# Kernel optimization log

Measured on AMD Instinct MI355X. Metric: run time of the kernel, lower is better.

## Reference

```python
import jax, jax.numpy as jnp
import numpy as np

B = 4096
FEAT = 40960
HID = 1024
L1 = 64
L2 = 32
P_ACTIVE = 30.0 / FEAT  # ~30 active features per position


def setup_inputs() -> dict:
    key = jax.random.key(0)
    ks = jax.random.split(key, 12)
    # Sparse binary HalfKP-style features
    white_features = (jax.random.uniform(ks[0], (B, FEAT)) < P_ACTIVE).astype(jnp.float32)
    black_features = (jax.random.uniform(ks[1], (B, FEAT)) < P_ACTIVE).astype(jnp.float32)
    stm = (jax.random.uniform(ks[2], (B, 1)) < 0.5).astype(jnp.float32)
    s = 0.02
    params = {
        'ft_w': jax.random.normal(ks[3], (HID, FEAT), jnp.float32) * s,
        'ft_b': jax.random.normal(ks[4], (HID,), jnp.float32) * s,
        'l1_w': jax.random.normal(ks[5], (L1, 2 * HID), jnp.float32) * s,
        'l1_b': jax.random.normal(ks[6], (L1,), jnp.float32) * s,
        'l2_w': jax.random.normal(ks[7], (L2, L1), jnp.float32) * s,
        'l2_b': jax.random.normal(ks[8], (L2,), jnp.float32) * s,
        'l3_w': jax.random.normal(ks[9], (1, L2), jnp.float32) * s,
        'l3_b': jax.random.normal(ks[10], (1,), jnp.float32) * s,
    }
    return dict(white_features=white_features, black_features=black_features, stm=stm, **params)


def reference(white_features, black_features, stm,
              ft_w, ft_b, l1_w, l1_b, l2_w, l2_b, l3_w, l3_b):
    # Feature transformer (shared weights, both perspectives)
    w = white_features @ ft_w.T + ft_b  # [B, HID]
    b = black_features @ ft_w.T + ft_b  # [B, HID]
    wb = jnp.concatenate([w, b], axis=1)  # [B, 2*HID]
    bw = jnp.concatenate([b, w], axis=1)
    acc = stm * wb + (1.0 - stm) * bw
    h1 = jnp.clip(acc, 0.0, 1.0)
    h2 = jnp.clip(h1 @ l1_w.T + l1_b, 0.0, 1.0)
    h3 = jnp.clip(h2 @ l2_w.T + l2_b, 0.0, 1.0)
    raw = h3 @ l3_w.T + l3_b  # [B, 1]
    return jax.nn.sigmoid(raw), raw
```

## Files before the change

### kernel.cpp

```cpp
#include <hip/hip_runtime.h>
#include <hip/hip_bf16.h>

#define B_SZ 4096
#define FEAT 40960
#define HID  1024
#define L1N  64
#define L2N  32
#define IDX_CAP 128
#define ROWS 4

static __device__ __forceinline__ unsigned short f2bf(float x) {
    __hip_bfloat16 h = __float2bfloat16(x);
    return *reinterpret_cast<unsigned short*>(&h);
}
static __device__ __forceinline__ float bf2f(unsigned short u) {
    unsigned int v = ((unsigned int)u) << 16;
    return __uint_as_float(v);
}
static __device__ __forceinline__ float bf2f_lo(unsigned int u) {
    return __uint_as_float(u << 16);
}
static __device__ __forceinline__ float bf2f_hi(unsigned int u) {
    return __uint_as_float(u & 0xffff0000u);
}
static __device__ __forceinline__ unsigned int packbf(float lo, float hi) {
    return (unsigned int)f2bf(lo) | ((unsigned int)f2bf(hi) << 16);
}
static __device__ __forceinline__ float clipf(float x) {
    return fminf(fmaxf(x, 0.0f), 1.0f);
}

__global__ __launch_bounds__(256) void transpose_ftw(
    const float* __restrict__ ftw, unsigned short* __restrict__ ftwT) {
    __shared__ float tile[32][65];
    const int tx = threadIdx.x;
    const int ty = threadIdx.y;
    const int f0 = blockIdx.x * 32;
    const int h0 = blockIdx.y * 64;
#pragma unroll
    for (int i = 0; i < 8; ++i) {
        int h = ty + 8 * i;
        tile[tx][h] = ftw[(size_t)(h0 + h) * FEAT + f0 + tx];
    }
    __syncthreads();
#pragma unroll
    for (int i = 0; i < 4; ++i) {
        int f = ty + 8 * i;
        unsigned int pk = packbf(tile[f][2 * tx], tile[f][2 * tx + 1]);
        ((unsigned int*)(ftwT + (size_t)(f0 + f) * HID + h0))[tx] = pk;
    }
}

__global__ __launch_bounds__(256) void scan_kernel(
    const float* __restrict__ wf, const float* __restrict__ bfeat,
    int* __restrict__ idx_ws, int* __restrict__ cnt_ws) {
    __shared__ int cnt;
    const int t = threadIdx.x;
    const int b = blockIdx.x;
    const int persp = b >> 12;
    const int row   = b & (B_SZ - 1);
    const float4* s4 = (const float4*)((persp ? bfeat : wf) + (size_t)row * FEAT);
    int* dst = idx_ws + (size_t)b * IDX_CAP;

    if (t == 0) cnt = 0;
    __syncthreads();

#pragma unroll 4
    for (int it = 0; it < (FEAT / 4) / 256; ++it) {
        int i4 = it * 256 + t;
        float4 v = s4[i4];
        int base = i4 * 4;
        if (v.x != 0.f) { int p = atomicAdd(&cnt, 1); if (p < IDX_CAP) dst[p] = base + 0; }
        if (v.y != 0.f) { int p = atomicAdd(&cnt, 1); if (p < IDX_CAP) dst[p] = base + 1; }
        if (v.z != 0.f) { int p = atomicAdd(&cnt, 1); if (p < IDX_CAP) dst[p] = base + 2; }
        if (v.w != 0.f) { int p = atomicAdd(&cnt, 1); if (p < IDX_CAP) dst[p] = base + 3; }
    }
    __syncthreads();
    if (t == 0) cnt_ws[b] = min(cnt, IDX_CAP);
}

__global__ __launch_bounds__(256) void gather_mlp(
    const float* __restrict__ stm, const unsigned short* __restrict__ ftwT,
    const float* __restrict__ ftb,
    const int* __restrict__ idx_ws, const int* __restrict__ cnt_ws,
    const float* __restrict__ l1w, const float* __restrict__ l1b,
    const float* __restrict__ l2w, const float* __restrict__ l2b,
    const float* __restrict__ l3w, const float* __restrict__ l3b,
    float* __restrict__ out) {

    __shared__ int idxs[2 * ROWS][IDX_CAP];
    __shared__ int cnts[2 * ROWS];
    __shared__ unsigned int h1p[ROWS][HID];
    __shared__ float4 part[4 * L1N];
    __shared__ float h2s[ROWS][L1N];
    __shared__ float h3s[ROWS][L2N];

    const int t = threadIdx.x;
    const int r0 = blockIdx.x * ROWS;

    if (t < 2 * ROWS) {
        int pp = t >> 2, r = t & 3;
        cnts[t] = cnt_ws[pp * B_SZ + r0 + r];
    }
    for (int i = t; i < 2 * ROWS * IDX_CAP; i += 256) {
        int l = i >> 7;
        int pp = l >> 2, r = l & 3;
        idxs[l][i & (IDX_CAP - 1)] =
            idx_ws[(size_t)(pp * B_SZ + r0 + r) * IDX_CAP + (i & (IDX_CAP - 1))];
    }
    __syncthreads();

    float4 bias = ((const float4*)ftb)[t];
    float acc[2][ROWS][4];
#pragma unroll
    for (int pp = 0; pp < 2; ++pp)
#pragma unroll
        for (int r = 0; r < ROWS; ++r) {
            acc[pp][r][0] = bias.x; acc[pp][r][1] = bias.y;
            acc[pp][r][2] = bias.z; acc[pp][r][3] = bias.w;
        }

#pragma unroll
    for (int pp = 0; pp < 2; ++pp)
#pragma unroll
        for (int r = 0; r < ROWS; ++r) {
            const int n = cnts[pp * ROWS + r];
            float* a = acc[pp][r];
#pragma unroll 4
            for (int i = 0; i < n; ++i) {
                int f = idxs[pp * ROWS + r][i];
                ushort4 u = ((const ushort4*)(ftwT + (size_t)f * HID))[t];
                a[0] += bf2f(u.x); a[1] += bf2f(u.y);
                a[2] += bf2f(u.z); a[3] += bf2f(u.w);
            }
        }

#pragma unroll
    for (int r = 0; r < ROWS; ++r) {
        const bool wfirst = (stm[r0 + r] != 0.0f);
        const float* fw = acc[0][r];
        const float* fb = acc[1][r];
        float f0 = wfirst ? fw[0] : fb[0], f1 = wfirst ? fw[1] : fb[1];
        float f2 = wfirst ? fw[2] : fb[2], f3 = wfirst ? fw[3] : fb[3];
        float s0 = wfirst ? fb[0] : fw[0], s1 = wfirst ? fb[1] : fw[1];
        float s2 = wfirst ? fb[2] : fw[2], s3 = wfirst ? fb[3] : fw[3];
        h1p[r][2 * t]           = packbf(clipf(f0), clipf(f1));
        h1p[r][2 * t + 1]       = packbf(clipf(f2), clipf(f3));
        h1p[r][512 + 2 * t]     = packbf(clipf(s0), clipf(s1));
        h1p[r][512 + 2 * t + 1] = packbf(clipf(s2), clipf(s3));
    }
    __syncthreads();

    {
        const int k = t & 63, p = t >> 6;
        float a0 = 0.f, a1 = 0.f, a2 = 0.f, a3 = 0.f;
        const float4* w4 = (const float4*)(l1w + (size_t)k * 2 * HID + (size_t)p * 512);
        const int qbase = p * 256;
        for (int jj = 0; jj < 128; ++jj) {
            float4 w = w4[jj];
            int q = qbase + 2 * jj;
            unsigned int u00 = h1p[0][q], u01 = h1p[0][q + 1];
            unsigned int u10 = h1p[1][q], u11 = h1p[1][q + 1];
            unsigned int u20 = h1p[2][q], u21 = h1p[2][q + 1];
            unsigned int u30 = h1p[3][q], u31 = h1p[3][q + 1];
            a0 += w.x * bf2f_lo(u00) + w.y * bf2f_hi(u00) + w.z * bf2f_lo(u01) + w.w * bf2f_hi(u01);
            a1 += w.x * bf2f_lo(u10) + w.y * bf2f_hi(u10) + w.z * bf2f_lo(u11) + w.w * bf2f_hi(u11);
            a2 += w.x * bf2f_lo(u20) + w.y * bf2f_hi(u20) + w.z * bf2f_lo(u21) + w.w * bf2f_hi(u21);
            a3 += w.x * bf2f_lo(u30) + w.y * bf2f_hi(u30) + w.z * bf2f_lo(u31) + w.w * bf2f_hi(u31);
        }
        part[p * L1N + k] = make_float4(a0, a1, a2, a3);
    }
    __syncthreads();
    if (t < L1N) {
        float4 s0 = part[t], s1 = part[L1N + t], s2 = part[2 * L1N + t], s3 = part[3 * L1N + t];
        float b1 = l1b[t];
        h2s[0][t] = clipf(s0.x + s1.x + s2.x + s3.x + b1);
        h2s[1][t] = clipf(s0.y + s1.y + s2.y + s3.y + b1);
        h2s[2][t] = clipf(s0.z + s1.z + s2.z + s3.z + b1);
        h2s[3][t] = clipf(s0.w + s1.w + s2.w + s3.w + b1);
    }
    __syncthreads();

    if (t < ROWS * L2N) {
        int r = t >> 5, k2 = t & 31;
        float a = l2b[k2];
        for (int j = 0; j < L1N; ++j) a += h2s[r][j] * l2w[k2 * L1N + j];
        h3s[r][k2] = clipf(a);
    }
    __syncthreads();

    if (t < ROWS) {
        float raw = l3b[0];
        for (int j = 0; j < L2N; ++j) raw += h3s[t][j] * l3w[j];
        out[r0 + t] = 1.0f / (1.0f + expf(-raw));
        out[B_SZ + r0 + t] = raw;
    }
}

extern "C" void kernel_launch(void* const* d_in, const int* in_sizes, int n_in,
                              void* d_out, int out_size, void* d_ws, size_t ws_size,
                              hipStream_t stream) {
    const float* wf    = (const float*)d_in[0];
    const float* bfeat = (const float*)d_in[1];
    const float* stm   = (const float*)d_in[2];
    const float* ftw   = (const float*)d_in[3];
    const float* ftb   = (const float*)d_in[4];
    const float* l1w   = (const float*)d_in[5];
    const float* l1b   = (const float*)d_in[6];
    const float* l2w   = (const float*)d_in[7];
    const float* l2b   = (const float*)d_in[8];
    const float* l3w   = (const float*)d_in[9];
    const float* l3b   = (const float*)d_in[10];
    float* out = (float*)d_out;

    unsigned short* ftwT = (unsigned short*)d_ws;
    int* idx_ws = (int*)(ftwT + (size_t)FEAT * HID);
    int* cnt_ws = idx_ws + (size_t)2 * B_SZ * IDX_CAP;

    transpose_ftw<<<dim3(FEAT / 32, HID / 64), dim3(32, 8), 0, stream>>>(ftw, ftwT);
    scan_kernel<<<2 * B_SZ, 256, 0, stream>>>(wf, bfeat, idx_ws, cnt_ws);
    gather_mlp<<<B_SZ / ROWS, 256, 0, stream>>>(stm, ftwT, ftb, idx_ws, cnt_ws,
                                                l1w, l1b, l2w, l2b, l3w, l3b, out);
}
```

Before: 1.459 ms.

## Fuse feature scan with embedding gather per row, split MLP into separate kernel

The sparse-index scan and the feature-transformer gather now run in one kernel, with one block per batch row. Indices stay in shared memory instead of going through a global workspace. Each block writes the clipped bf16 h1 activations to global memory, and a separate MLP kernel loads them in 4-row tiles. This drops the index workspace round trip, raises gather parallelism from 1024 blocks to 4096, and lets scan and gather work from different blocks overlap. The cost is an extra kernel launch and a global write and read of h1.

New measurement: 1.451 ms. About the same (-0.5%).

```diff
diff --git a/kernel.cpp b/kernel.cpp
--- a/kernel.cpp
+++ b/kernel.cpp
@@ -14,8 +14,7 @@
     return *reinterpret_cast<unsigned short*>(&h);
 }
 static __device__ __forceinline__ float bf2f(unsigned short u) {
-    unsigned int v = ((unsigned int)u) << 16;
-    return __uint_as_float(v);
+    return __uint_as_float(((unsigned int)u) << 16);
 }
 static __device__ __forceinline__ float bf2f_lo(unsigned int u) {
     return __uint_as_float(u << 16);
@@ -51,45 +50,77 @@
     }
 }
 
-__global__ __launch_bounds__(256) void scan_kernel(
+__global__ __launch_bounds__(256) void scan_gather(
     const float* __restrict__ wf, const float* __restrict__ bfeat,
-    int* __restrict__ idx_ws, int* __restrict__ cnt_ws) {
-    __shared__ int cnt;
+    const float* __restrict__ stm, const unsigned short* __restrict__ ftwT,
+    const float* __restrict__ ftb, unsigned int* __restrict__ h1) {
+
+    __shared__ int idxs[2][IDX_CAP];
+    __shared__ int cnts[2];
+
     const int t = threadIdx.x;
-    const int b = blockIdx.x;
-    const int persp = b >> 12;
-    const int row   = b & (B_SZ - 1);
-    const float4* s4 = (const float4*)((persp ? bfeat : wf) + (size_t)row * FEAT);
-    int* dst = idx_ws + (size_t)b * IDX_CAP;
-
-    if (t == 0) cnt = 0;
-    __syncthreads();
-
+    const int row = blockIdx.x;
+
+    if (t < 2) cnts[t] = 0;
+    __syncthreads();
+
+#pragma unroll
+    for (int pp = 0; pp < 2; ++pp) {
+        const float4* s4 = (const float4*)((pp ? bfeat : wf) + (size_t)row * FEAT);
 #pragma unroll 4
-    for (int it = 0; it < (FEAT / 4) / 256; ++it) {
-        int i4 = it * 256 + t;
-        float4 v = s4[i4];
-        int base = i4 * 4;
-        if (v.x != 0.f) { int p = atomicAdd(&cnt, 1); if (p < IDX_CAP) dst[p] = base + 0; }
-        if (v.y != 0.f) { int p = atomicAdd(&cnt, 1); if (p < IDX_CAP) dst[p] = base + 1; }
-        if (v.z != 0.f) { int p = atomicAdd(&cnt, 1); if (p < IDX_CAP) dst[p] = base + 2; }
-        if (v.w != 0.f) { int p = atomicAdd(&cnt, 1); if (p < IDX_CAP) dst[p] = base + 3; }
-    }
-    __syncthreads();
-    if (t == 0) cnt_ws[b] = min(cnt, IDX_CAP);
-}
-
-__global__ __launch_bounds__(256) void gather_mlp(
-    const float* __restrict__ stm, const unsigned short* __restrict__ ftwT,
-    const float* __restrict__ ftb,
-    const int* __restrict__ idx_ws, const int* __restrict__ cnt_ws,
+        for (int it = 0; it < (FEAT / 4) / 256; ++it) {
+            int i4 = it * 256 + t;
+            float4 v = s4[i4];
+            int base = i4 * 4;
+            if (v.x != 0.f) { int p = atomicAdd(&cnts[pp], 1); if (p < IDX_CAP) idxs[pp][p] = base + 0; }
+            if (v.y != 0.f) { int p = atomicAdd(&cnts[pp], 1); if (p < IDX_CAP) idxs[pp][p] = base + 1; }
+            if (v.z != 0.f) { int p = atomicAdd(&cnts[pp], 1); if (p < IDX_CAP) idxs[pp][p] = base + 2; }
+            if (v.w != 0.f) { int p = atomicAdd(&cnts[pp], 1); if (p < IDX_CAP) idxs[pp][p] = base + 3; }
+        }
+    }
+    __syncthreads();
+
+    const int nw = min(cnts[0], IDX_CAP);
+    const int nb = min(cnts[1], IDX_CAP);
+    float4 bias = ((const float4*)ftb)[t];
+    float aw0 = bias.x, aw1 = bias.y, aw2 = bias.z, aw3 = bias.w;
+    float ab0 = bias.x, ab1 = bias.y, ab2 = bias.z, ab3 = bias.w;
+
+#pragma unroll 4
+    for (int i = 0; i < nw; ++i) {
+        int f = idxs[0][i];
+        ushort4 u = ((const ushort4*)(ftwT + (size_t)f * HID))[t];
+        aw0 += bf2f(u.x); aw1 += bf2f(u.y); aw2 += bf2f(u.z); aw3 += bf2f(u.w);
+    }
+#pragma unroll 4
+    for (int i = 0; i < nb; ++i) {
+        int f = idxs[1][i];
+        ushort4 u = ((const ushort4*)(ftwT + (size_t)f * HID))[t];
+        ab0 += bf2f(u.x); ab1 += bf2f(u.y); ab2 += bf2f(u.z); ab3 += bf2f(u.w);
+    }
+
+    const bool wfirst = (stm[row] != 0.0f);
+    float f0 = wfirst ? aw0 : ab0, f1 = wfirst ? aw1 : ab1;
+    float f2 = wfirst ? aw2 : ab2, f3 = wfirst ? aw3 : ab3;
+    float s0 = wfirst ? ab0 : aw0, s1 = wfirst ? ab1 : aw1;
+    float s2 = wfirst ? ab2 : aw2, s3 = wfirst ? ab3 : aw3;
+
+    uint2 pf, ps;
+    pf.x = packbf(clipf(f0), clipf(f1)); pf.y = packbf(clipf(f2), clipf(f3));
+    ps.x = packbf(clipf(s0), clipf(s1)); ps.y = packbf(clipf(s2), clipf(s3));
+
+    unsigned int* dst = h1 + (size_t)row * (2 * HID / 2);
+    ((uint2*)dst)[t]                 = pf;
+    ((uint2*)(dst + HID / 2 * 1))[t + 0] = ps;
+}
+
+__global__ __launch_bounds__(256) void mlp_kernel(
+    const unsigned int* __restrict__ h1,
     const float* __restrict__ l1w, const float* __restrict__ l1b,
     const float* __restrict__ l2w, const float* __restrict__ l2b,
     const float* __restrict__ l3w, const float* __restrict__ l3b,
     float* __restrict__ out) {
 
-    __shared__ int idxs[2 * ROWS][IDX_CAP];
-    __shared__ int cnts[2 * ROWS];
     __shared__ unsigned int h1p[ROWS][HID];
     __shared__ float4 part[4 * L1N];
     __shared__ float h2s[ROWS][L1N];
@@ -98,56 +129,11 @@
     const int t = threadIdx.x;
     const int r0 = blockIdx.x * ROWS;
 
-    if (t < 2 * ROWS) {
-        int pp = t >> 2, r = t & 3;
-        cnts[t] = cnt_ws[pp * B_SZ + r0 + r];
-    }
-    for (int i = t; i < 2 * ROWS * IDX_CAP; i += 256) {
-        int l = i >> 7;
-        int pp = l >> 2, r = l & 3;
-        idxs[l][i & (IDX_CAP - 1)] =
-            idx_ws[(size_t)(pp * B_SZ + r0 + r) * IDX_CAP + (i & (IDX_CAP - 1))];
-    }
-    __syncthreads();
-
-    float4 bias = ((const float4*)ftb)[t];
-    float acc[2][ROWS][4];
-#pragma unroll
-    for (int pp = 0; pp < 2; ++pp)
-#pragma unroll
-        for (int r = 0; r < ROWS; ++r) {
-            acc[pp][r][0] = bias.x; acc[pp][r][1] = bias.y;
-            acc[pp][r][2] = bias.z; acc[pp][r][3] = bias.w;
-        }
-
-#pragma unroll
-    for (int pp = 0; pp < 2; ++pp)
-#pragma unroll
-        for (int r = 0; r < ROWS; ++r) {
-            const int n = cnts[pp * ROWS + r];
-            float* a = acc[pp][r];
-#pragma unroll 4
-            for (int i = 0; i < n; ++i) {
-                int f = idxs[pp * ROWS + r][i];
-                ushort4 u = ((const ushort4*)(ftwT + (size_t)f * HID))[t];
-                a[0] += bf2f(u.x); a[1] += bf2f(u.y);
-                a[2] += bf2f(u.z); a[3] += bf2f(u.w);
-            }
-        }
-
-#pragma unroll
-    for (int r = 0; r < ROWS; ++r) {
-        const bool wfirst = (stm[r0 + r] != 0.0f);
-        const float* fw = acc[0][r];
-        const float* fb = acc[1][r];
-        float f0 = wfirst ? fw[0] : fb[0], f1 = wfirst ? fw[1] : fb[1];
-        float f2 = wfirst ? fw[2] : fb[2], f3 = wfirst ? fw[3] : fb[3];
-        float s0 = wfirst ? fb[0] : fw[0], s1 = wfirst ? fb[1] : fw[1];
-        float s2 = wfirst ? fb[2] : fw[2], s3 = wfirst ? fb[3] : fw[3];
-        h1p[r][2 * t]           = packbf(clipf(f0), clipf(f1));
-        h1p[r][2 * t + 1]       = packbf(clipf(f2), clipf(f3));
-        h1p[r][512 + 2 * t]     = packbf(clipf(s0), clipf(s1));
-        h1p[r][512 + 2 * t + 1] = packbf(clipf(s2), clipf(s3));
+    {
+        const uint4* src = (const uint4*)(h1 + (size_t)r0 * HID);
+        uint4* dst = (uint4*)&h1p[0][0];
+#pragma unroll
+        for (int i = 0; i < 4; ++i) dst[i * 256 + t] = src[i * 256 + t];
     }
     __syncthreads();
 
@@ -214,11 +200,9 @@
     float* out = (float*)d_out;
 
     unsigned short* ftwT = (unsigned short*)d_ws;
-    int* idx_ws = (int*)(ftwT + (size_t)FEAT * HID);
-    int* cnt_ws = idx_ws + (size_t)2 * B_SZ * IDX_CAP;
+    unsigned int* h1 = (unsigned int*)(ftwT + (size_t)FEAT * HID);
 
     transpose_ftw<<<dim3(FEAT / 32, HID / 64), dim3(32, 8), 0, stream>>>(ftw, ftwT);
-    scan_kernel<<<2 * B_SZ, 256, 0, stream>>>(wf, bfeat, idx_ws, cnt_ws);
-    gather_mlp<<<B_SZ / ROWS, 256, 0, stream>>>(stm, ftwT, ftb, idx_ws, cnt_ws,
-                                                l1w, l1b, l2w, l2b, l3w, l3b, out);
-}
+    scan_gather<<<B_SZ, 256, 0, stream>>>(wf, bfeat, stm, ftwT, ftb, h1);
+    mlp_kernel<<<B_SZ / ROWS, 256, 0, stream>>>(h1, l1w, l1b, l2w, l2b, l3w, l3b, out);
+}
```
